# Optimization experiments

Hardware: AMD Instinct MI355X
Metric: run time of the kernel (lower is better)

Reference implementation:

```python
import jax, jax.numpy as jnp
import numpy as np

B, N = 64, 200000
R = 4                 # voxel_resolution
V = R ** 3            # flattened voxel grid size
CLASSES = 40


def setup_inputs() -> dict:
    key = jax.random.key(0)
    k1, k2 = jax.random.split(key, 2)
    x = jax.random.normal(k1, (B, N, 3), dtype=jnp.float32)
    # Linear(V, CLASSES) parameters
    W = jax.random.normal(k2, (CLASSES, V), dtype=jnp.float32) * 0.05
    b = jnp.zeros((CLASSES,), dtype=jnp.float32)
    return {"x": x, "W": W, "b": b}


def _voxel_counts(x):
    # histogramdd over range [-R/2, R/2] per dim with R bins -> bin width 1
    lo = -R / 2.0
    hi = R / 2.0
    # points outside [lo, hi] on any dim are dropped (histogramdd semantics);
    # points exactly at hi fall into the last bin (rightmost edge inclusive)
    inside = jnp.all((x >= lo) & (x <= hi), axis=-1)          # [B, N]
    idx = jnp.clip(jnp.floor(x - lo).astype(jnp.int32), 0, R - 1)  # [B, N, 3]
    flat = idx[..., 0] * (R * R) + idx[..., 1] * R + idx[..., 2]   # [B, N]
    seg = jnp.arange(B, dtype=jnp.int32)[:, None] * V + flat       # [B, N]
    w = inside.astype(jnp.float32)
    counts = jax.ops.segment_sum(w.ravel(), seg.ravel(), num_segments=B * V)
    counts = counts.reshape(B, V)
    counts = counts / counts.sum(axis=1, keepdims=True)  # fraction of in-range points
    return counts


def reference(x, W, b):
    counts = _voxel_counts(x)               # [B, V]
    return counts @ W.T + b                 # [B, CLASSES]
```

## Files before the change

### kernel.cpp

```cpp
#include <hip/hip_runtime.h>

#define TPB 256
#define BPB 16

__global__ __launch_bounds__(TPB) void hist_kernel(const float* __restrict__ x,
                                                   unsigned* __restrict__ counts,
                                                   int N) {
    __shared__ unsigned h[64];
    if (threadIdx.x < 64) h[threadIdx.x] = 0u;
    __syncthreads();

    const int b = blockIdx.y;
    const float* xb = x + (size_t)b * (size_t)N * 3u;
    const int chunk = (N + gridDim.x - 1) / gridDim.x;
    const int start = blockIdx.x * chunk;
    const int end   = min(N, start + chunk);

    for (int i = start + (int)threadIdx.x; i < end; i += TPB) {
        const float x0 = xb[3 * i + 0];
        const float x1 = xb[3 * i + 1];
        const float x2 = xb[3 * i + 2];
        const bool inside = (x0 >= -2.0f) & (x0 <= 2.0f) &
                            (x1 >= -2.0f) & (x1 <= 2.0f) &
                            (x2 >= -2.0f) & (x2 <= 2.0f);
        const int i0 = min(3, max(0, (int)floorf(x0 + 2.0f)));
        const int i1 = min(3, max(0, (int)floorf(x1 + 2.0f)));
        const int i2 = min(3, max(0, (int)floorf(x2 + 2.0f)));
        if (inside) atomicAdd(&h[(i0 << 4) | (i1 << 2) | i2], 1u);
    }
    __syncthreads();

    if (threadIdx.x < 64) {
        const unsigned v = h[threadIdx.x];
        if (v) atomicAdd(&counts[b * 64 + threadIdx.x], v);
    }
}

__global__ __launch_bounds__(64) void linear_kernel(const unsigned* __restrict__ counts,
                                                    const float* __restrict__ W,
                                                    const float* __restrict__ bias,
                                                    float* __restrict__ out) {
    const int b = blockIdx.x;
    __shared__ float cnt[64];
    cnt[threadIdx.x] = (float)counts[b * 64 + threadIdx.x];
    __syncthreads();

    const int c = threadIdx.x;
    if (c < 40) {
        float acc = 0.0f, tot = 0.0f;
        #pragma unroll
        for (int v = 0; v < 64; ++v) {
            const float cv = cnt[v];
            tot += cv;
            acc = fmaf(cv, W[c * 64 + v], acc);
        }
        out[b * 40 + c] = acc / tot + bias[c];
    }
}

extern "C" void kernel_launch(void* const* d_in, const int* in_sizes, int n_in,
                              void* d_out, int out_size, void* d_ws, size_t ws_size,
                              hipStream_t stream) {
    const float* x    = (const float*)d_in[0];
    const float* W    = (const float*)d_in[1];
    const float* bias = (const float*)d_in[2];
    float* out = (float*)d_out;

    const int B = 64;
    const int N = in_sizes[0] / (B * 3);

    unsigned* counts = (unsigned*)d_ws;
    hipMemsetAsync(counts, 0, (size_t)B * 64 * sizeof(unsigned), stream);

    dim3 grid(BPB, B);
    hist_kernel<<<grid, TPB, 0, stream>>>(x, counts, N);
    linear_kernel<<<B, 64, 0, stream>>>(counts, W, bias, out);
}
```

Baseline: 226.7 us.

## Vectorize histogram loads with float4 nontemporal reads and double blocks per batch

Each thread now reads 4 points (12 floats) as three 16-byte nontemporal vector loads in a grid-strided loop, instead of three scalar strided loads per point. The block count per batch goes from 16 to 32 and the range check is simplified to fabsf comparisons with float clamping. A tail loop in block 0 handles N not divisible by 4. The goal is better memory bandwidth utilisation on a purely bandwidth-bound 153 MB read; it relies on each batch's base being 16-byte aligned, which holds because N is divisible by 4.

```diff
diff --git a/kernel.cpp b/kernel.cpp
--- a/kernel.cpp
+++ b/kernel.cpp
@@ -1,10 +1,13 @@
 #include <hip/hip_runtime.h>
 
 #define TPB 256
-#define BPB 16
+#define BPB 32
+
+typedef float floatx4 __attribute__((ext_vector_type(4)));
 
 __global__ __launch_bounds__(TPB) void hist_kernel(const float* __restrict__ x,
                                                    unsigned* __restrict__ counts,
+                                                   int Q,
                                                    int N) {
     __shared__ unsigned h[64];
     if (threadIdx.x < 64) h[threadIdx.x] = 0u;
@@ -12,21 +15,31 @@
 
     const int b = blockIdx.y;
     const float* xb = x + (size_t)b * (size_t)N * 3u;
-    const int chunk = (N + gridDim.x - 1) / gridDim.x;
-    const int start = blockIdx.x * chunk;
-    const int end   = min(N, start + chunk);
+    const floatx4* xq = (const floatx4*)xb;
 
-    for (int i = start + (int)threadIdx.x; i < end; i += TPB) {
-        const float x0 = xb[3 * i + 0];
-        const float x1 = xb[3 * i + 1];
-        const float x2 = xb[3 * i + 2];
-        const bool inside = (x0 >= -2.0f) & (x0 <= 2.0f) &
-                            (x1 >= -2.0f) & (x1 <= 2.0f) &
-                            (x2 >= -2.0f) & (x2 <= 2.0f);
-        const int i0 = min(3, max(0, (int)floorf(x0 + 2.0f)));
-        const int i1 = min(3, max(0, (int)floorf(x1 + 2.0f)));
-        const int i2 = min(3, max(0, (int)floorf(x2 + 2.0f)));
+    auto process = [&](float a, float bb, float c) {
+        const bool inside = (fabsf(a) <= 2.0f) & (fabsf(bb) <= 2.0f) & (fabsf(c) <= 2.0f);
+        const int i0 = (int)fminf(fmaxf(floorf(a  + 2.0f), 0.0f), 3.0f);
+        const int i1 = (int)fminf(fmaxf(floorf(bb + 2.0f), 0.0f), 3.0f);
+        const int i2 = (int)fminf(fmaxf(floorf(c  + 2.0f), 0.0f), 3.0f);
         if (inside) atomicAdd(&h[(i0 << 4) | (i1 << 2) | i2], 1u);
+    };
+
+    const int stride = gridDim.x * TPB;
+    for (int q = blockIdx.x * TPB + (int)threadIdx.x; q < Q; q += stride) {
+        const floatx4 p0 = __builtin_nontemporal_load(&xq[3 * q + 0]);
+        const floatx4 p1 = __builtin_nontemporal_load(&xq[3 * q + 1]);
+        const floatx4 p2 = __builtin_nontemporal_load(&xq[3 * q + 2]);
+        process(p0.x, p0.y, p0.z);
+        process(p0.w, p1.x, p1.y);
+        process(p1.z, p1.w, p2.x);
+        process(p2.y, p2.z, p2.w);
+    }
+
+    if (blockIdx.x == 0) {
+        for (int i = 4 * Q + (int)threadIdx.x; i < N; i += TPB) {
+            process(xb[3 * i], xb[3 * i + 1], xb[3 * i + 2]);
+        }
     }
     __syncthreads();
 
@@ -68,11 +81,12 @@
 
     const int B = 64;
     const int N = in_sizes[0] / (B * 3);
+    const int Q = N / 4;
 
     unsigned* counts = (unsigned*)d_ws;
-    hipMemsetAsync(counts, 0, (size_t)B * 64 * sizeof(unsigned), stream);
+    (void)hipMemsetAsync(counts, 0, (size_t)B * 64 * sizeof(unsigned), stream);
 
     dim3 grid(BPB, B);
-    hist_kernel<<<grid, TPB, 0, stream>>>(x, counts, N);
+    hist_kernel<<<grid, TPB, 0, stream>>>(x, counts, Q, N);
     linear_kernel<<<B, 64, 0, stream>>>(counts, W, bias, out);
 }
```

Result: faster. 222.1 us (-2.0%).
